# Kernel optimization log

Measured on AMD Instinct MI355X. Metric: run time of the kernel, lower is better.

## Reference

```python
import jax, jax.numpy as jnp
import numpy as np

NHEAD = 16
FREQ = 10000.0


def rope(x, freq=FREQ):
    # x: [B, S, D]; rotary applied over the FULL feature dim (pre head-split),
    # pairing even/odd channels, matching the original module's op order.
    B, S, D = x.shape
    inv_freq = freq ** (-jnp.arange(0, D, 2, dtype=jnp.float32) / D)  # [D/2]
    ang = jnp.arange(S, dtype=jnp.float32)[:, None] * inv_freq[None, :]  # [S, D/2]
    cos, sin = jnp.cos(ang), jnp.sin(ang)
    x1, x2 = x[..., 0::2], x[..., 1::2]
    out_even = x1 * cos - x2 * sin
    out_odd = x1 * sin + x2 * cos
    return jnp.stack([out_even, out_odd], axis=-1).reshape(B, S, D)


def setup_inputs() -> dict:
    key = jax.random.key(0)
    ks = jax.random.split(key, 9)
    B, S, D = 4, 2048, 1024
    sc = 1.0 / np.sqrt(D)
    return {
        "queries": jax.random.normal(ks[0], (B, S, D), jnp.float32),
        "Wq": jax.random.normal(ks[1], (D, D), jnp.float32) * sc,
        "bq": jnp.zeros((D,), jnp.float32),
        "Wk": jax.random.normal(ks[2], (D, D), jnp.float32) * sc,
        "bk": jnp.zeros((D,), jnp.float32),
        "Wv": jax.random.normal(ks[3], (D, D), jnp.float32) * sc,
        "bv": jnp.zeros((D,), jnp.float32),
        "Wo": jax.random.normal(ks[4], (D, D), jnp.float32) * sc,
        "bo": jnp.zeros((D,), jnp.float32),
    }


def reference(queries, Wq, bq, Wk, bk, Wv, bv, Wo, bo):
    B, S, D = queries.shape
    H = NHEAD
    dh = D // H
    # self-attention: values = keys = queries
    q = rope(queries @ Wq.T + bq)
    k = rope(queries @ Wk.T + bk)
    v = queries @ Wv.T + bv
    # separate heads: [B, S, D] -> [B, H, S, dh]
    q = q.reshape(B, S, H, dh).transpose(0, 2, 1, 3)
    k = k.reshape(B, S, H, dh).transpose(0, 2, 1, 3)
    v = v.reshape(B, S, H, dh).transpose(0, 2, 1, 3)
    scores = jnp.einsum("bhqd,bhkd->bhqk", q, k) / jnp.sqrt(jnp.float32(dh))
    attn = jax.nn.softmax(scores, axis=-1)
    heads = jnp.einsum("bhqk,bhkd->bhqd", attn, v)
    out = heads.transpose(0, 2, 1, 3).reshape(B, S, D)
    return out @ Wo.T + bo
```

## Files before the change

### kernel.cpp

```cpp
#include <hip/hip_runtime.h>
#include <stdint.h>

typedef __bf16 bf16_t;
typedef __bf16 bf16x4 __attribute__((ext_vector_type(4)));
typedef __bf16 bf16x8 __attribute__((ext_vector_type(8)));
typedef float  f32x4  __attribute__((ext_vector_type(4)));

#define BB   4
#define SS   2048
#define DD   1024
#define HH   16
#define DH   64

#if __has_builtin(__builtin_amdgcn_exp2f)
#define EXP2F(x) __builtin_amdgcn_exp2f(x)
#else
#define EXP2F(x) __expf((x) * 0.6931471805599453f)
#endif

__device__ __forceinline__ void gload_lds16(const void* g, void* l) {
    __builtin_amdgcn_global_load_lds(
        (__attribute__((address_space(1))) void*)(uintptr_t)g,
        (__attribute__((address_space(3))) void*)(uint32_t)(uintptr_t)l,
        16, 0, 0);
}

__global__ __launch_bounds__(256) void prep_kernel(
        const float* __restrict__ queries,
        const float* __restrict__ Wq, const float* __restrict__ Wk,
        const float* __restrict__ Wv, const float* __restrict__ Wo,
        const float* __restrict__ bq, const float* __restrict__ bk,
        const float* __restrict__ bv,
        bf16_t* __restrict__ Xb, bf16_t* __restrict__ Wqkv,
        bf16_t* __restrict__ Wob, float* __restrict__ bqkv,
        float2* __restrict__ tab)
{
    const int bid = blockIdx.x, t = threadIdx.x;
    if (bid < 8192) {
        const int i = bid * 256 + t;
        float4 v = ((const float4*)queries)[i];
        bf16x4 o;
        o.x = (bf16_t)v.x; o.y = (bf16_t)v.y; o.z = (bf16_t)v.z; o.w = (bf16_t)v.w;
        ((bf16x4*)Xb)[i] = o;
    } else if (bid < 12288) {
        const int i = (bid - 8192) * 256 + t;
        const int which = i >> 18, p = i & 262143;
        const float* src = (which == 0) ? Wq : (which == 1) ? Wk : (which == 2) ? Wv : Wo;
        bf16_t* dst = (which < 3) ? (Wqkv + (long)which * 1048576) : Wob;
        float4 v = ((const float4*)src)[p];
        bf16x4 o;
        o.x = (bf16_t)v.x; o.y = (bf16_t)v.y; o.z = (bf16_t)v.z; o.w = (bf16_t)v.w;
        ((bf16x4*)dst)[p] = o;
    } else if (bid < 16384) {
        const int i = (bid - 12288) * 256 + t;
        const int s = i >> 9, pr = i & 511;
        float inv = powf(10000.0f, -(float)(2 * pr) * (1.0f / 1024.0f));
        float c, sn;
        sincosf((float)s * inv, &sn, &c);
        tab[i] = make_float2(c, sn);
    } else {
        const int i = (bid - 16384) * 256 + t;
        if (i < 3072)
            bqkv[i] = (i < 1024) ? bq[i] : ((i < 2048) ? bk[i - 1024] : bv[i - 2048]);
    }
}

__global__ __launch_bounds__(256, 2) void gemm_qkv_rope(
        const bf16_t* __restrict__ A, const bf16_t* __restrict__ Bm,
        const float* __restrict__ bias, const float2* __restrict__ tab,
        bf16_t* __restrict__ Qb, bf16_t* __restrict__ Kb, bf16_t* __restrict__ Vtmp)
{
    __shared__ __attribute__((aligned(16))) bf16_t As[128 * 32];
    __shared__ __attribute__((aligned(16))) bf16_t Bs[128 * 32];
    const int t = threadIdx.x;
    const int lane = t & 63, w = t >> 6;
    const int wm = w >> 1, wn = w & 1;
    const int l15 = lane & 15, l4 = lane >> 4;
    const long rowA0 = (long)blockIdx.x * 128;
    const long rowB0 = (long)blockIdx.y * 128;
    const int K = 1024, N = 1024;

    const f32x4 vz = {0.f, 0.f, 0.f, 0.f};
    f32x4 acc[4][4];
#pragma unroll
    for (int i = 0; i < 4; ++i)
#pragma unroll
        for (int j = 0; j < 4; ++j) acc[i][j] = vz;

    for (int kk = 0; kk < K; kk += 32) {
        __syncthreads();
#pragma unroll
        for (int i = 0; i < 2; ++i) {
            const int cb = i * 256 + w * 64;
            const int c  = cb + lane;
            const int r  = c >> 2;
            const int ko = (c & 3) << 3;
            gload_lds16(A  + (rowA0 + r) * K + kk + ko, As + cb * 8);
            gload_lds16(Bm + (rowB0 + r) * K + kk + ko, Bs + cb * 8);
        }
        __syncthreads();
        bf16x8 af[4], bfr[4];
#pragma unroll
        for (int i = 0; i < 4; ++i)
            af[i] = *(const bf16x8*)(As + (wm * 64 + i * 16 + l15) * 32 + l4 * 8);
#pragma unroll
        for (int j = 0; j < 4; ++j)
            bfr[j] = *(const bf16x8*)(Bs + (wn * 64 + j * 16 + l15) * 32 + l4 * 8);
#pragma unroll
        for (int i = 0; i < 4; ++i)
#pragma unroll
            for (int j = 0; j < 4; ++j)
                acc[i][j] = __builtin_amdgcn_mfma_f32_16x16x32_bf16(af[i], bfr[j], acc[i][j], 0, 0, 0);
    }

    const long crow0 = rowA0 + wm * 64;
    const int  ccol0 = (int)rowB0 + wn * 64;
    const int  part  = blockIdx.y >> 3;

    if (part == 2) {
#pragma unroll
        for (int i = 0; i < 4; ++i) {
#pragma unroll
            for (int j = 0; j < 4; ++j) {
                const int col = ccol0 + j * 16 + l15;
                const float bb = bias[col];
                const int vc = col - 2048;
#pragma unroll
                for (int r = 0; r < 4; ++r) {
                    const long row = crow0 + i * 16 + l4 * 4 + r;
                    Vtmp[row * N + vc] = (bf16_t)(acc[i][j][r] + bb);
                }
            }
        }
    } else {
        bf16_t* dst0 = part ? Kb : Qb;
        const int h = (ccol0 & 1023) >> 6;
#pragma unroll
        for (int i = 0; i < 4; ++i) {
#pragma unroll
            for (int j = 0; j < 4; ++j) {
                const int col = ccol0 + j * 16 + l15;
                const float bb = bias[col];
                const int even = !(col & 1);
                const int dd = j * 16 + l15;
                const float2* trow = tab + (col >> 1 & 511);
#pragma unroll
                for (int r = 0; r < 4; ++r) {
                    const long row = crow0 + i * 16 + l4 * 4 + r;
                    const int b = (int)(row >> 11), s = (int)(row & 2047);
                    const float val = acc[i][j][r] + bb;
                    const float par = __shfl_xor(val, 1);
                    const float2 cs = trow[s * 512];
                    const float out = even ? (val * cs.x - par * cs.y)
                                           : fmaf(val, cs.x, par * cs.y);
                    dst0[((long)((b * HH + h) * SS + s)) * DH + dd] = (bf16_t)out;
                }
            }
        }
    }
}

template <int OUT_BF16>
__global__ __launch_bounds__(256, 2) void gemm_bt(
        const bf16_t* __restrict__ A, const bf16_t* __restrict__ Bm,
        const float* __restrict__ bias, void* __restrict__ Cout,
        int M, int N, int K)
{
    __shared__ __attribute__((aligned(16))) bf16_t As[128 * 32];
    __shared__ __attribute__((aligned(16))) bf16_t Bs[128 * 32];
    const int t = threadIdx.x;
    const int lane = t & 63, w = t >> 6;
    const int wm = w >> 1, wn = w & 1;
    const int l15 = lane & 15, l4 = lane >> 4;
    const long rowA0 = (long)blockIdx.x * 128;
    const long rowB0 = (long)blockIdx.y * 128;

    const f32x4 vz = {0.f, 0.f, 0.f, 0.f};
    f32x4 acc[4][4];
#pragma unroll
    for (int i = 0; i < 4; ++i)
#pragma unroll
        for (int j = 0; j < 4; ++j) acc[i][j] = vz;

    for (int kk = 0; kk < K; kk += 32) {
        __syncthreads();
#pragma unroll
        for (int i = 0; i < 2; ++i) {
            const int cb = i * 256 + w * 64;
            const int c  = cb + lane;
            const int r  = c >> 2;
            const int ko = (c & 3) << 3;
            gload_lds16(A  + (rowA0 + r) * K + kk + ko, As + cb * 8);
            gload_lds16(Bm + (rowB0 + r) * K + kk + ko, Bs + cb * 8);
        }
        __syncthreads();
        bf16x8 af[4], bfr[4];
#pragma unroll
        for (int i = 0; i < 4; ++i)
            af[i] = *(const bf16x8*)(As + (wm * 64 + i * 16 + l15) * 32 + l4 * 8);
#pragma unroll
        for (int j = 0; j < 4; ++j)
            bfr[j] = *(const bf16x8*)(Bs + (wn * 64 + j * 16 + l15) * 32 + l4 * 8);
#pragma unroll
        for (int i = 0; i < 4; ++i)
#pragma unroll
            for (int j = 0; j < 4; ++j)
                acc[i][j] = __builtin_amdgcn_mfma_f32_16x16x32_bf16(af[i], bfr[j], acc[i][j], 0, 0, 0);
    }

    const long crow0 = rowA0 + wm * 64;
    const int  ccol0 = (int)rowB0 + wn * 64;
#pragma unroll
    for (int i = 0; i < 4; ++i) {
#pragma unroll
        for (int j = 0; j < 4; ++j) {
            const int col = ccol0 + j * 16 + l15;
            const float bb = bias[col];
#pragma unroll
            for (int r = 0; r < 4; ++r) {
                const long row = crow0 + i * 16 + l4 * 4 + r;
                const float v = acc[i][j][r] + bb;
                if (OUT_BF16) ((bf16_t*)Cout)[row * N + col] = (bf16_t)v;
                else          ((float*)Cout)[row * N + col]  = v;
            }
        }
    }
}

__global__ __launch_bounds__(256) void repack_v(const bf16_t* __restrict__ Vtmp,
                                                bf16_t* __restrict__ Vt)
{
    __shared__ bf16_t tile[64][66];
    const int t = threadIdx.x;
    const int st = blockIdx.x, bh = blockIdx.y;
    const int b = bh >> 4, h = bh & 15;
    const long nbase = (long)b * SS + st * 64;
    const int rr = t >> 3, c8 = (t & 7) * 8;
#pragma unroll
    for (int e = 0; e < 2; ++e) {
        const int r = e * 32 + rr;
        union { bf16x8 v; unsigned int u[4]; } ld;
        ld.v = *(const bf16x8*)(Vtmp + (nbase + r) * 1024 + h * 64 + c8);
#pragma unroll
        for (int k = 0; k < 4; ++k)
            *(unsigned int*)(&tile[r][c8 + 2 * k]) = ld.u[k];
    }
    __syncthreads();
#pragma unroll
    for (int e = 0; e < 2; ++e) {
        const int d = e * 32 + rr;
        bf16x8 o;
#pragma unroll
        for (int k = 0; k < 8; ++k) o[k] = tile[c8 + k][d];
        *(bf16x8*)(Vt + ((long)bh * DH + d) * SS + st * 64 + c8) = o;
    }
}

__global__ __launch_bounds__(256, 3) void attn_kernel(const bf16_t* __restrict__ Qb,
                                                      const bf16_t* __restrict__ Kb,
                                                      const bf16_t* __restrict__ Vt,
                                                      bf16_t* __restrict__ Ob)
{
    __shared__ __attribute__((aligned(16))) bf16_t Ks[2][64 * 64];
    __shared__ __attribute__((aligned(16))) bf16_t Vs[2][64 * 64];
    __shared__ __attribute__((aligned(16))) bf16_t Ps[128 * 72];
    const int t = threadIdx.x, lane = t & 63, w = t >> 6;
    const int l15 = lane & 15, l4 = lane >> 4;
    const int xr = l15 & 7;
    const int qt = blockIdx.x, bh = blockIdx.y;
    const bf16_t* Qbh = Qb + (long)bh * SS * DH;
    const bf16_t* Kbh = Kb + (long)bh * SS * DH;
    const bf16_t* Vbh = Vt + (long)bh * DH * SS;

    const int qbase = qt * 128 + w * 32;
    bf16x8 qf[2][2];
#pragma unroll
    for (int s = 0; s < 2; ++s) {
        const long qrow = qbase + 16 * s + l15;
        qf[s][0] = *(const bf16x8*)(Qbh + qrow * DH + l4 * 8);
        qf[s][1] = *(const bf16x8*)(Qbh + qrow * DH + 32 + l4 * 8);
    }

    const f32x4 vz = {0.f, 0.f, 0.f, 0.f};
    f32x4 oacc[2][4];
#pragma unroll
    for (int s = 0; s < 2; ++s)
#pragma unroll
        for (int j = 0; j < 4; ++j) oacc[s][j] = vz;
    float l_sum[2] = {0.f, 0.f};

    int srow[2], scc[2];
#pragma unroll
    for (int i = 0; i < 2; ++i) {
        const int L = i * 256 + w * 64 + lane;
        srow[i] = L >> 3;
        scc[i]  = (L & 7) ^ (srow[i] & 7);
    }

    const float SC = 0.125f * 1.4426950408889634f;
    const float BI = -8.0f  * 1.4426950408889634f;

    auto stage = [&](int kt, int buf) {
        const bf16_t* Ksrc = Kbh + (long)kt * 64 * DH;
#pragma unroll
        for (int i = 0; i < 2; ++i) {
            const int cb = i * 256 + w * 64;
            gload_lds16(Ksrc + srow[i] * 64 + scc[i] * 8, &Ks[buf][cb * 8]);
            gload_lds16(Vbh + (long)srow[i] * SS + kt * 64 + scc[i] * 8, &Vs[buf][cb * 8]);
        }
    };

    stage(0, 0);
    __syncthreads();

    for (int kt = 0; kt < SS / 64; ++kt) {
        const int p = kt & 1;
        if (kt + 1 < SS / 64) stage(kt + 1, p ^ 1);
        const bf16_t* KsP = Ks[p];
        const bf16_t* VsP = Vs[p];

        f32x4 sacc[2][4];
#pragma unroll
        for (int s = 0; s < 2; ++s)
#pragma unroll
            for (int j = 0; j < 4; ++j) sacc[s][j] = vz;
#pragma unroll
        for (int j = 0; j < 4; ++j) {
            const int rk = (j * 16 + l15) * 64;
            const bf16x8 kf0 = *(const bf16x8*)(KsP + rk + ((l4 ^ xr) * 8));
            const bf16x8 kf1 = *(const bf16x8*)(KsP + rk + (((4 + l4) ^ xr) * 8));
#pragma unroll
            for (int s = 0; s < 2; ++s) {
                sacc[s][j] = __builtin_amdgcn_mfma_f32_16x16x32_bf16(kf0, qf[s][0], sacc[s][j], 0, 0, 0);
                sacc[s][j] = __builtin_amdgcn_mfma_f32_16x16x32_bf16(kf1, qf[s][1], sacc[s][j], 0, 0, 0);
            }
        }

#pragma unroll
        for (int s = 0; s < 2; ++s) {
#pragma unroll
            for (int j = 0; j < 4; ++j) {
                const float p0 = EXP2F(fmaf(sacc[s][j][0], SC, BI));
                const float p1 = EXP2F(fmaf(sacc[s][j][1], SC, BI));
                const float p2 = EXP2F(fmaf(sacc[s][j][2], SC, BI));
                const float p3 = EXP2F(fmaf(sacc[s][j][3], SC, BI));
                l_sum[s] += (p0 + p1) + (p2 + p3);
                bf16x4 pk;
                pk.x = (bf16_t)p0; pk.y = (bf16_t)p1; pk.z = (bf16_t)p2; pk.w = (bf16_t)p3;
                *(bf16x4*)(Ps + (w * 32 + 16 * s + l15) * 72 + j * 16 + l4 * 4) = pk;
            }
        }

        bf16x8 pf[2][2];
#pragma unroll
        for (int s = 0; s < 2; ++s) {
            pf[s][0] = *(const bf16x8*)(Ps + (w * 32 + 16 * s + l15) * 72 + l4 * 8);
            pf[s][1] = *(const bf16x8*)(Ps + (w * 32 + 16 * s + l15) * 72 + 32 + l4 * 8);
        }
#pragma unroll
        for (int j = 0; j < 4; ++j) {
            const int rv = (j * 16 + l15) * 64;
            const bf16x8 vf0 = *(const bf16x8*)(VsP + rv + ((l4 ^ xr) * 8));
            const bf16x8 vf1 = *(const bf16x8*)(VsP + rv + (((4 + l4) ^ xr) * 8));
#pragma unroll
            for (int s = 0; s < 2; ++s) {
                oacc[s][j] = __builtin_amdgcn_mfma_f32_16x16x32_bf16(pf[s][0], vf0, oacc[s][j], 0, 0, 0);
                oacc[s][j] = __builtin_amdgcn_mfma_f32_16x16x32_bf16(pf[s][1], vf1, oacc[s][j], 0, 0, 0);
            }
        }

        __syncthreads();
    }

    const int b = bh >> 4, h = bh & 15;
#pragma unroll
    for (int s = 0; s < 2; ++s) {
        float lt = l_sum[s];
        lt += __shfl_xor(lt, 16);
        lt += __shfl_xor(lt, 32);
        const float inv = 1.0f / lt;
        float invr[4];
#pragma unroll
        for (int r = 0; r < 4; ++r)
            invr[r] = __shfl(inv, l4 * 4 + r);
#pragma unroll
        for (int j = 0; j < 4; ++j) {
#pragma unroll
            for (int r = 0; r < 4; ++r) {
                const int row = qbase + 16 * s + l4 * 4 + r;
                const float v = oacc[s][j][r] * invr[r];
                Ob[((long)(b * SS + row)) * DD + h * DH + j * 16 + l15] = (bf16_t)v;
            }
        }
    }
}

extern "C" void kernel_launch(void* const* d_in, const int* in_sizes, int n_in,
                              void* d_out, int out_size, void* d_ws, size_t ws_size,
                              hipStream_t stream)
{
    const float* queries = (const float*)d_in[0];
    const float* Wq = (const float*)d_in[1];
    const float* bq = (const float*)d_in[2];
    const float* Wk = (const float*)d_in[3];
    const float* bk = (const float*)d_in[4];
    const float* Wv = (const float*)d_in[5];
    const float* bv = (const float*)d_in[6];
    const float* Wo = (const float*)d_in[7];
    const float* bo = (const float*)d_in[8];

    char* ws = (char*)d_ws;
    size_t off = 0;
    auto alloc = [&](size_t bytes) { size_t o = off; off += (bytes + 255) & ~(size_t)255; return o; };
    bf16_t* Xb   = (bf16_t*)(ws + alloc(8192u * 1024u * 2u));
    bf16_t* Wqkv = (bf16_t*)(ws + alloc(3072u * 1024u * 2u));
    bf16_t* Wob  = (bf16_t*)(ws + alloc(1024u * 1024u * 2u));
    float*  bqkv = (float*) (ws + alloc(3072u * 4u));
    float2* tab  = (float2*)(ws + alloc(2048u * 512u * 8u));
    bf16_t* Vtmp = (bf16_t*)(ws + alloc(8192u * 1024u * 2u));
    bf16_t* Qb   = (bf16_t*)(ws + alloc(64u * 2048u * 64u * 2u));
    bf16_t* Kb   = (bf16_t*)(ws + alloc(64u * 2048u * 64u * 2u));
    bf16_t* Vt   = (bf16_t*)(ws + alloc(64u * 64u * 2048u * 2u));
    bf16_t* Ob   = Xb;

    prep_kernel<<<16396, 256, 0, stream>>>(queries, Wq, Wk, Wv, Wo, bq, bk, bv,
                                           Xb, Wqkv, Wob, bqkv, tab);

    gemm_qkv_rope<<<dim3(64, 24), 256, 0, stream>>>(Xb, Wqkv, bqkv, tab, Qb, Kb, Vtmp);
    repack_v<<<dim3(32, 64), 256, 0, stream>>>(Vtmp, Vt);
    attn_kernel<<<dim3(16, 64), 256, 0, stream>>>(Qb, Kb, Vt, Ob);
    gemm_bt<0><<<dim3(64, 8), 256, 0, stream>>>(Ob, Wob, bo, d_out, 8192, 1024, 1024);
}
```

Before: 301.5 us.

## Fuse V transpose into QKV GEMM, swizzle GEMM LDS, single-buffer attention

The QKV GEMM epilogue now writes V directly in transposed per-head layout as packed 4-element vectors, removing the separate repack kernel and its intermediate buffer. Q/K stores are paired via a lane shuffle into 32-bit writes. GEMM LDS tiles get an XOR swizzle on the k-chunk to reduce bank conflicts, and launch bounds rise to 3 blocks per CU. The attention kernel drops double buffering for a single LDS buffer with occupancy 4. This loses load/compute overlap in attention in exchange for higher occupancy.

New measurement: 300.3 us. No clear change (-0.4%).

```diff
diff --git a/kernel.cpp b/kernel.cpp
--- a/kernel.cpp
+++ b/kernel.cpp
@@ -65,10 +65,10 @@
     }
 }
 
-__global__ __launch_bounds__(256, 2) void gemm_qkv_rope(
+__global__ __launch_bounds__(256, 3) void gemm_qkv_rope(
         const bf16_t* __restrict__ A, const bf16_t* __restrict__ Bm,
         const float* __restrict__ bias, const float2* __restrict__ tab,
-        bf16_t* __restrict__ Qb, bf16_t* __restrict__ Kb, bf16_t* __restrict__ Vtmp)
+        bf16_t* __restrict__ Qb, bf16_t* __restrict__ Kb, bf16_t* __restrict__ Vt)
 {
     __shared__ __attribute__((aligned(16))) bf16_t As[128 * 32];
     __shared__ __attribute__((aligned(16))) bf16_t Bs[128 * 32];
@@ -76,9 +76,10 @@
     const int lane = t & 63, w = t >> 6;
     const int wm = w >> 1, wn = w & 1;
     const int l15 = lane & 15, l4 = lane >> 4;
+    const int xg = l15 & 3;
     const long rowA0 = (long)blockIdx.x * 128;
     const long rowB0 = (long)blockIdx.y * 128;
-    const int K = 1024, N = 1024;
+    const int K = 1024;
 
     const f32x4 vz = {0.f, 0.f, 0.f, 0.f};
     f32x4 acc[4][4];
@@ -94,7 +95,7 @@
             const int cb = i * 256 + w * 64;
             const int c  = cb + lane;
             const int r  = c >> 2;
-            const int ko = (c & 3) << 3;
+            const int ko = ((c & 3) ^ (r & 3)) << 3;
             gload_lds16(A  + (rowA0 + r) * K + kk + ko, As + cb * 8);
             gload_lds16(Bm + (rowB0 + r) * K + kk + ko, Bs + cb * 8);
         }
@@ -102,10 +103,10 @@
         bf16x8 af[4], bfr[4];
 #pragma unroll
         for (int i = 0; i < 4; ++i)
-            af[i] = *(const bf16x8*)(As + (wm * 64 + i * 16 + l15) * 32 + l4 * 8);
+            af[i] = *(const bf16x8*)(As + (wm * 64 + i * 16 + l15) * 32 + ((l4 ^ xg) * 8));
 #pragma unroll
         for (int j = 0; j < 4; ++j)
-            bfr[j] = *(const bf16x8*)(Bs + (wn * 64 + j * 16 + l15) * 32 + l4 * 8);
+            bfr[j] = *(const bf16x8*)(Bs + (wn * 64 + j * 16 + l15) * 32 + ((l4 ^ xg) * 8));
 #pragma unroll
         for (int i = 0; i < 4; ++i)
 #pragma unroll
@@ -116,44 +117,52 @@
     const long crow0 = rowA0 + wm * 64;
     const int  ccol0 = (int)rowB0 + wn * 64;
     const int  part  = blockIdx.y >> 3;
+    const int  b     = (int)(crow0 >> 11);
+    const int  s0    = (int)(crow0 & 2047);
 
     if (part == 2) {
+        const int h = (ccol0 - 2048) >> 6;
+#pragma unroll
+        for (int j = 0; j < 4; ++j) {
+            const int d = j * 16 + l15;
+            const float bb = bias[ccol0 + j * 16 + l15];
+            bf16_t* dstc = Vt + ((long)(b * HH + h) * DH + d) * SS + s0;
+#pragma unroll
+            for (int i = 0; i < 4; ++i) {
+                bf16x4 pk;
+                pk.x = (bf16_t)(acc[i][j][0] + bb);
+                pk.y = (bf16_t)(acc[i][j][1] + bb);
+                pk.z = (bf16_t)(acc[i][j][2] + bb);
+                pk.w = (bf16_t)(acc[i][j][3] + bb);
+                *(bf16x4*)(dstc + i * 16 + l4 * 4) = pk;
+            }
+        }
+    } else {
+        bf16_t* dst0 = part ? Kb : Qb;
+        const int h = (ccol0 & 1023) >> 6;
+        const int even = !(l15 & 1);
 #pragma unroll
         for (int i = 0; i < 4; ++i) {
 #pragma unroll
             for (int j = 0; j < 4; ++j) {
                 const int col = ccol0 + j * 16 + l15;
                 const float bb = bias[col];
-                const int vc = col - 2048;
-#pragma unroll
-                for (int r = 0; r < 4; ++r) {
-                    const long row = crow0 + i * 16 + l4 * 4 + r;
-                    Vtmp[row * N + vc] = (bf16_t)(acc[i][j][r] + bb);
-                }
-            }
-        }
-    } else {
-        bf16_t* dst0 = part ? Kb : Qb;
-        const int h = (ccol0 & 1023) >> 6;
-#pragma unroll
-        for (int i = 0; i < 4; ++i) {
-#pragma unroll
-            for (int j = 0; j < 4; ++j) {
-                const int col = ccol0 + j * 16 + l15;
-                const float bb = bias[col];
-                const int even = !(col & 1);
                 const int dd = j * 16 + l15;
                 const float2* trow = tab + (col >> 1 & 511);
 #pragma unroll
                 for (int r = 0; r < 4; ++r) {
-                    const long row = crow0 + i * 16 + l4 * 4 + r;
-                    const int b = (int)(row >> 11), s = (int)(row & 2047);
+                    const int s = s0 + i * 16 + l4 * 4 + r;
                     const float val = acc[i][j][r] + bb;
                     const float par = __shfl_xor(val, 1);
                     const float2 cs = trow[s * 512];
                     const float out = even ? (val * cs.x - par * cs.y)
                                            : fmaf(val, cs.x, par * cs.y);
-                    dst0[((long)((b * HH + h) * SS + s)) * DH + dd] = (bf16_t)out;
+                    const float op = __shfl_xor(out, 1);
+                    if (even) {
+                        union { bf16_t hh[2]; unsigned int u; } cv;
+                        cv.hh[0] = (bf16_t)out; cv.hh[1] = (bf16_t)op;
+                        *(unsigned int*)(dst0 + ((long)((b * HH + h) * SS + s)) * DH + dd) = cv.u;
+                    }
                 }
             }
         }
@@ -161,7 +170,7 @@
 }
 
 template <int OUT_BF16>
-__global__ __launch_bounds__(256, 2) void gemm_bt(
+__global__ __launch_bounds__(256, 3) void gemm_bt(
         const bf16_t* __restrict__ A, const bf16_t* __restrict__ Bm,
         const float* __restrict__ bias, void* __restrict__ Cout,
         int M, int N, int K)
@@ -172,6 +181,7 @@
     const int lane = t & 63, w = t >> 6;
     const int wm = w >> 1, wn = w & 1;
     const int l15 = lane & 15, l4 = lane >> 4;
+    const int xg = l15 & 3;
     const long rowA0 = (long)blockIdx.x * 128;
     const long rowB0 = (long)blockIdx.y * 128;
 
@@ -189,7 +199,7 @@
             const int cb = i * 256 + w * 64;
             const int c  = cb + lane;
             const int r  = c >> 2;
-            const int ko = (c & 3) << 3;
+            const int ko = ((c & 3) ^ (r & 3)) << 3;
             gload_lds16(A  + (rowA0 + r) * K + kk + ko, As + cb * 8);
             gload_lds16(Bm + (rowB0 + r) * K + kk + ko, Bs + cb * 8);
         }
@@ -197,10 +207,10 @@
         bf16x8 af[4], bfr[4];
 #pragma unroll
         for (int i = 0; i < 4; ++i)
-            af[i] = *(const bf16x8*)(As + (wm * 64 + i * 16 + l15) * 32 + l4 * 8);
+            af[i] = *(const bf16x8*)(As + (wm * 64 + i * 16 + l15) * 32 + ((l4 ^ xg) * 8));
 #pragma unroll
         for (int j = 0; j < 4; ++j)
-            bfr[j] = *(const bf16x8*)(Bs + (wn * 64 + j * 16 + l15) * 32 + l4 * 8);
+            bfr[j] = *(const bf16x8*)(Bs + (wn * 64 + j * 16 + l15) * 32 + ((l4 ^ xg) * 8));
 #pragma unroll
         for (int i = 0; i < 4; ++i)
 #pragma unroll
@@ -227,42 +237,13 @@
     }
 }
 
-__global__ __launch_bounds__(256) void repack_v(const bf16_t* __restrict__ Vtmp,
-                                                bf16_t* __restrict__ Vt)
-{
-    __shared__ bf16_t tile[64][66];
-    const int t = threadIdx.x;
-    const int st = blockIdx.x, bh = blockIdx.y;
-    const int b = bh >> 4, h = bh & 15;
-    const long nbase = (long)b * SS + st * 64;
-    const int rr = t >> 3, c8 = (t & 7) * 8;
-#pragma unroll
-    for (int e = 0; e < 2; ++e) {
-        const int r = e * 32 + rr;
-        union { bf16x8 v; unsigned int u[4]; } ld;
-        ld.v = *(const bf16x8*)(Vtmp + (nbase + r) * 1024 + h * 64 + c8);
-#pragma unroll
-        for (int k = 0; k < 4; ++k)
-            *(unsigned int*)(&tile[r][c8 + 2 * k]) = ld.u[k];
-    }
-    __syncthreads();
-#pragma unroll
-    for (int e = 0; e < 2; ++e) {
-        const int d = e * 32 + rr;
-        bf16x8 o;
-#pragma unroll
-        for (int k = 0; k < 8; ++k) o[k] = tile[c8 + k][d];
-        *(bf16x8*)(Vt + ((long)bh * DH + d) * SS + st * 64 + c8) = o;
-    }
-}
-
-__global__ __launch_bounds__(256, 3) void attn_kernel(const bf16_t* __restrict__ Qb,
+__global__ __launch_bounds__(256, 4) void attn_kernel(const bf16_t* __restrict__ Qb,
                                                       const bf16_t* __restrict__ Kb,
                                                       const bf16_t* __restrict__ Vt,
                                                       bf16_t* __restrict__ Ob)
 {
-    __shared__ __attribute__((aligned(16))) bf16_t Ks[2][64 * 64];
-    __shared__ __attribute__((aligned(16))) bf16_t Vs[2][64 * 64];
+    __shared__ __attribute__((aligned(16))) bf16_t Ks[64 * 64];
+    __shared__ __attribute__((aligned(16))) bf16_t Vs[64 * 64];
     __shared__ __attribute__((aligned(16))) bf16_t Ps[128 * 72];
     const int t = threadIdx.x, lane = t & 63, w = t >> 6;
     const int l15 = lane & 15, l4 = lane >> 4;
@@ -300,24 +281,16 @@
     const float SC = 0.125f * 1.4426950408889634f;
     const float BI = -8.0f  * 1.4426950408889634f;
 
-    auto stage = [&](int kt, int buf) {
+    for (int kt = 0; kt < SS / 64; ++kt) {
+        __syncthreads();
         const bf16_t* Ksrc = Kbh + (long)kt * 64 * DH;
 #pragma unroll
         for (int i = 0; i < 2; ++i) {
             const int cb = i * 256 + w * 64;
-            gload_lds16(Ksrc + srow[i] * 64 + scc[i] * 8, &Ks[buf][cb * 8]);
-            gload_lds16(Vbh + (long)srow[i] * SS + kt * 64 + scc[i] * 8, &Vs[buf][cb * 8]);
-        }
-    };
-
-    stage(0, 0);
-    __syncthreads();
-
-    for (int kt = 0; kt < SS / 64; ++kt) {
-        const int p = kt & 1;
-        if (kt + 1 < SS / 64) stage(kt + 1, p ^ 1);
-        const bf16_t* KsP = Ks[p];
-        const bf16_t* VsP = Vs[p];
+            gload_lds16(Ksrc + srow[i] * 64 + scc[i] * 8, Ks + cb * 8);
+            gload_lds16(Vbh + (long)srow[i] * SS + kt * 64 + scc[i] * 8, Vs + cb * 8);
+        }
+        __syncthreads();
 
         f32x4 sacc[2][4];
 #pragma unroll
@@ -327,8 +300,8 @@
 #pragma unroll
         for (int j = 0; j < 4; ++j) {
             const int rk = (j * 16 + l15) * 64;
-            const bf16x8 kf0 = *(const bf16x8*)(KsP + rk + ((l4 ^ xr) * 8));
-            const bf16x8 kf1 = *(const bf16x8*)(KsP + rk + (((4 + l4) ^ xr) * 8));
+            const bf16x8 kf0 = *(const bf16x8*)(Ks + rk + ((l4 ^ xr) * 8));
+            const bf16x8 kf1 = *(const bf16x8*)(Ks + rk + (((4 + l4) ^ xr) * 8));
 #pragma unroll
             for (int s = 0; s < 2; ++s) {
                 sacc[s][j] = __builtin_amdgcn_mfma_f32_16x16x32_bf16(kf0, qf[s][0], sacc[s][j], 0, 0, 0);
@@ -360,16 +333,14 @@
 #pragma unroll
         for (int j = 0; j < 4; ++j) {
             const int rv = (j * 16 + l15) * 64;
-            const bf16x8 vf0 = *(const bf16x8*)(VsP + rv + ((l4 ^ xr) * 8));
-            const bf16x8 vf1 = *(const bf16x8*)(VsP + rv + (((4 + l4) ^ xr) * 8));
+            const bf16x8 vf0 = *(const bf16x8*)(Vs + rv + ((l4 ^ xr) * 8));
+            const bf16x8 vf1 = *(const bf16x8*)(Vs + rv + (((4 + l4) ^ xr) * 8));
 #pragma unroll
             for (int s = 0; s < 2; ++s) {
                 oacc[s][j] = __builtin_amdgcn_mfma_f32_16x16x32_bf16(pf[s][0], vf0, oacc[s][j], 0, 0, 0);
                 oacc[s][j] = __builtin_amdgcn_mfma_f32_16x16x32_bf16(pf[s][1], vf1, oacc[s][j], 0, 0, 0);
             }
         }
-
-        __syncthreads();
     }
 
     const int b = bh >> 4, h = bh & 15;
@@ -417,7 +388,6 @@
     bf16_t* Wob  = (bf16_t*)(ws + alloc(1024u * 1024u * 2u));
     float*  bqkv = (float*) (ws + alloc(3072u * 4u));
     float2* tab  = (float2*)(ws + alloc(2048u * 512u * 8u));
-    bf16_t* Vtmp = (bf16_t*)(ws + alloc(8192u * 1024u * 2u));
     bf16_t* Qb   = (bf16_t*)(ws + alloc(64u * 2048u * 64u * 2u));
     bf16_t* Kb   = (bf16_t*)(ws + alloc(64u * 2048u * 64u * 2u));
     bf16_t* Vt   = (bf16_t*)(ws + alloc(64u * 64u * 2048u * 2u));
@@ -426,8 +396,7 @@
     prep_kernel<<<16396, 256, 0, stream>>>(queries, Wq, Wk, Wv, Wo, bq, bk, bv,
                                            Xb, Wqkv, Wob, bqkv, tab);
 
-    gemm_qkv_rope<<<dim3(64, 24), 256, 0, stream>>>(Xb, Wqkv, bqkv, tab, Qb, Kb, Vtmp);
-    repack_v<<<dim3(32, 64), 256, 0, stream>>>(Vtmp, Vt);
+    gemm_qkv_rope<<<dim3(64, 24), 256, 0, stream>>>(Xb, Wqkv, bqkv, tab, Qb, Kb, Vt);
     attn_kernel<<<dim3(16, 64), 256, 0, stream>>>(Qb, Kb, Vt, Ob);
     gemm_bt<0><<<dim3(64, 8), 256, 0, stream>>>(Ob, Wob, bo, d_out, 8192, 1024, 1024);
 }
```
